# Kernel optimization log

Measured on AMD Instinct MI355X. Metric: run time of the kernel, lower is better.

## Reference

```python
import jax, jax.numpy as jnp
import numpy as np

N, E, B = 4096, 8192, 128


def seg_softmax(logits, seg, n):
    m = jax.ops.segment_max(logits, seg, num_segments=n)
    e = jnp.exp(logits - m[seg])
    s = jax.ops.segment_sum(e, seg, num_segments=n)
    return e / (s[seg] + 1e-16)


def gat(x, src, dst, W, a_src, a_dst, b, H, C, n):
    # PyG GATConv, concat=False (mean over heads), self-loops already appended
    h = (x @ W).reshape(n, H, C)
    al_s = jnp.sum(h * a_src, -1)  # [n,H]
    al_d = jnp.sum(h * a_dst, -1)
    logits = jax.nn.leaky_relu(al_s[src] + al_d[dst], 0.2)  # [E',H]
    alpha = seg_softmax(logits, dst, n)
    out = jax.ops.segment_sum(h[src] * alpha[:, :, None], dst, num_segments=n)
    return out.mean(1) + b


def gcn(x, src, dst, W, b, n):
    deg = jax.ops.segment_sum(jnp.ones_like(dst, jnp.float32), dst, num_segments=n)
    dis = jnp.where(deg > 0, deg ** -0.5, 0.0)
    norm = dis[src] * dis[dst]
    h = x @ W
    return jax.ops.segment_sum(h[src] * norm[:, None], dst, num_segments=n) + b


def transformer_conv(x, src, dst, Wq, bq, Wk, bk, Wv, bv, Ws, bs, H, C, n):
    # PyG TransformerConv, concat=False, root_weight=True, no self-loops
    q = (x @ Wq + bq).reshape(n, H, C)
    k = (x @ Wk + bk).reshape(n, H, C)
    v = (x @ Wv + bv).reshape(n, H, C)
    logits = jnp.sum(q[dst] * k[src], -1) / jnp.sqrt(jnp.float32(C))  # [E,H]
    alpha = seg_softmax(logits, dst, n)
    agg = jax.ops.segment_sum(v[src] * alpha[:, :, None], dst, num_segments=n)
    return agg.mean(1) + (x @ Ws + bs)


def gap(x, batch, nb):
    s = jax.ops.segment_sum(x, batch, num_segments=nb)
    cnt = jax.ops.segment_sum(jnp.ones(x.shape[0], x.dtype), batch, num_segments=nb)
    return s / jnp.maximum(cnt, 1.0)[:, None]


def setup_inputs() -> dict:
    key = jax.random.key(0)
    ks = iter(jax.random.split(key, 64))
    p = {}
    p['x'] = jax.random.normal(next(ks), (N, 78), jnp.float32)
    p['fp'] = (jax.random.uniform(next(ks), (B, 1489)) > 0.5).astype(jnp.float32)
    p['edge_index'] = jax.random.randint(next(ks), (2, E), 0, N, jnp.int32)
    p['batch'] = (jnp.arange(N, dtype=jnp.int32) // (N // B))
    def w(k, shp, fan):
        return jax.random.normal(k, shp, jnp.float32) * (1.0 / np.sqrt(fan))
    # GAT layers (in, out, heads=8)
    for name, ci, co in [('g1', 78, 2048), ('g2', 2048, 1024), ('g3', 1024, 512)]:
        p[name + '_w'] = w(next(ks), (ci, 8 * co), ci)
        p[name + '_as'] = w(next(ks), (8, co), co)
        p[name + '_ad'] = w(next(ks), (8, co), co)
        p[name + '_b'] = jnp.zeros((co,), jnp.float32)
    p['gcn_w'] = w(next(ks), (512, 256), 512)
    p['gcn_b'] = jnp.zeros((256,), jnp.float32)
    # TransformerConv 78->512, heads=4
    for nm in ['t_wq', 't_wk', 't_wv']:
        p[nm] = w(next(ks), (78, 4 * 512), 78)
    for nm in ['t_bq', 't_bk', 't_bv']:
        p[nm] = jnp.zeros((4 * 512,), jnp.float32)
    p['t_ws'] = w(next(ks), (78, 512), 78)
    p['t_bs'] = jnp.zeros((512,), jnp.float32)
    p['fc1_w'] = w(next(ks), (1489, 128), 1489); p['fc1_b'] = jnp.zeros((128,), jnp.float32)
    p['fc2_w'] = w(next(ks), (128, 256), 128); p['fc2_b'] = jnp.zeros((256,), jnp.float32)
    for nm, ci, co in [('b1', 1024, 256), ('b2', 256, 128), ('b3', 128, 64), ('b4', 64, 1)]:
        p[nm + '_w'] = w(next(ks), (ci, co), ci)
        p[nm + '_b'] = jnp.zeros((co,), jnp.float32)
    return p


def reference(x, fp, edge_index, batch,
              g1_w, g1_as, g1_ad, g1_b, g2_w, g2_as, g2_ad, g2_b,
              g3_w, g3_as, g3_ad, g3_b, gcn_w, gcn_b,
              t_wq, t_wk, t_wv, t_bq, t_bk, t_bv, t_ws, t_bs,
              fc1_w, fc1_b, fc2_w, fc2_b,
              b1_w, b1_b, b2_w, b2_b, b3_w, b3_b, b4_w, b4_b):
    n = x.shape[0]
    sl = jnp.arange(n, dtype=edge_index.dtype)
    src_sl = jnp.concatenate([edge_index[0], sl])  # with self loops (GAT/GCN)
    dst_sl = jnp.concatenate([edge_index[1], sl])
    h = jax.nn.relu(gat(x, src_sl, dst_sl, g1_w, g1_as, g1_ad, g1_b, 8, 2048, n))
    h = jax.nn.relu(gat(h, src_sl, dst_sl, g2_w, g2_as, g2_ad, g2_b, 8, 1024, n))
    h = jax.nn.relu(gat(h, src_sl, dst_sl, g3_w, g3_as, g3_ad, g3_b, 8, 512, n))
    h = gcn(h, src_sl, dst_sl, gcn_w, gcn_b, n)
    x_gat = gap(h, batch, B)  # [B,256]
    fpn = jax.nn.relu(fp @ fc1_w + fc1_b)
    fpn = jax.nn.relu(fpn @ fc2_w + fc2_b)  # [B,256]
    xt = jax.nn.relu(transformer_conv(x, edge_index[0], edge_index[1],
                                      t_wq, t_bq, t_wk, t_bk, t_wv, t_bv,
                                      t_ws, t_bs, 4, 512, n))
    x_trans = gap(xt, batch, B)  # [B,512]
    xc = jnp.concatenate([x_gat, x_trans, fpn], axis=1)  # [B,1024]
    h = jax.nn.relu(xc @ b1_w + b1_b)
    h = jax.nn.relu(h @ b2_w + b2_b)
    h = jax.nn.relu(h @ b3_w + b3_b)
    return jax.nn.sigmoid(h @ b4_w + b4_b)
```

## Files before the change

### kernel.cpp

```cpp
#include <hip/hip_runtime.h>

typedef unsigned short u16;
typedef unsigned int   u32;

typedef __bf16 bf16x8 __attribute__((ext_vector_type(8)));
typedef float  f32x4  __attribute__((ext_vector_type(4)));

#define NNODE 4096
#define NEDGE 8192
#define NEG   12288

__device__ __forceinline__ float blo(u32 u){ return __uint_as_float(u<<16); }
__device__ __forceinline__ float bhi(u32 u){ return __uint_as_float(u & 0xffff0000u); }
__device__ __forceinline__ u16 f2b(float f){
  u32 u = __float_as_uint(f);
  u += 0x7fffu + ((u>>16)&1u);
  return (u16)(u>>16);
}
__device__ __forceinline__ void split_bf(float a, u16& hi, u16& lo){
  u32 u = __float_as_uint(a);
  u32 r = u + 0x7fffu + ((u>>16)&1u);
  hi = (u16)(r>>16);
  float h = __uint_as_float(r & 0xffff0000u);
  float l = a - h;
  u32 u2 = __float_as_uint(l);
  lo = (u16)((u2 + 0x7fffu + ((u2>>16)&1u)) >> 16);
}
__device__ __forceinline__ u16 hi_bf(float a){
  u32 u = __float_as_uint(a);
  return (u16)((u + 0x7fffu + ((u>>16)&1u)) >> 16);
}

#define GL2LDS(g,l) __builtin_amdgcn_global_load_lds((const __attribute__((address_space(1))) unsigned int*)(g), (__attribute__((address_space(3))) unsigned int*)(l), 16, 0, 0)

__global__ __launch_bounds__(256) void zero_i(int* p, int n){
  int i = blockIdx.x*256 + threadIdx.x; if (i<n) p[i]=0;
}
__global__ __launch_bounds__(256) void hist_k(const int* __restrict__ ei, int* deg_g, int* deg_t){
  int e = blockIdx.x*256 + threadIdx.x; if (e>=NEG) return;
  int dv = (e<NEDGE) ? ei[NEDGE+e] : e-NEDGE;
  atomicAdd(&deg_g[dv],1);
  if (e<NEDGE) atomicAdd(&deg_t[dv],1);
}
__global__ __launch_bounds__(1024) void scan4096(const int* __restrict__ deg, int* __restrict__ off){
  __shared__ int lds[1024];
  int tid = threadIdx.x;
  int v[4]; int s=0;
  #pragma unroll
  for (int j=0;j<4;j++){ v[j]=deg[tid*4+j]; s+=v[j]; }
  lds[tid]=s; __syncthreads();
  for (int d=1; d<1024; d<<=1){
    int t = (tid>=d) ? lds[tid-d] : 0;
    __syncthreads();
    lds[tid] += t;
    __syncthreads();
  }
  int base = (tid>0) ? lds[tid-1] : 0;
  #pragma unroll
  for (int j=0;j<4;j++){ off[tid*4+j]=base; base+=v[j]; }
  if (tid==1023) off[4096]=base;
}
__global__ __launch_bounds__(256) void scatter_k(const int* __restrict__ ei,
    const int* __restrict__ off_g, int* cur_g, int* csr_g,
    const int* __restrict__ off_t, int* cur_t, int* csr_t){
  int e = blockIdx.x*256 + threadIdx.x; if (e>=NEG) return;
  int s, dv;
  if (e<NEDGE){ s=ei[e]; dv=ei[NEDGE+e]; } else { s=dv=e-NEDGE; }
  int p = atomicAdd(&cur_g[dv],1);
  csr_g[off_g[dv]+p]=s;
  if (e<NEDGE){ int p2 = atomicAdd(&cur_t[dv],1); csr_t[off_t[dv]+p2]=s; }
}
__global__ __launch_bounds__(256) void mkdis(const int* __restrict__ deg, float* dis){
  int i = blockIdx.x*256 + threadIdx.x; if (i>=NNODE) return;
  int d = deg[i]; dis[i] = d>0 ? rsqrtf((float)d) : 0.f;
}
__global__ __launch_bounds__(128) void pad_x(const float* __restrict__ x, float* __restrict__ xp,
                                             u16* __restrict__ xh){
  int n = blockIdx.x, c = threadIdx.x;
  if (c<96){
    float v = (c<78) ? x[(size_t)n*78+c] : 0.f;
    if (c<80) xp[(size_t)n*80+c] = v;
    xh[(size_t)n*96+c] = hi_bf(v);
  }
}
__global__ __launch_bounds__(256) void repack_w1(const float* __restrict__ g1w, float* __restrict__ w1r){
  int i = blockIdx.x*256 + threadIdx.x;
  int kk = i >> 11, c = i & 2047;
  int h = kk/80, k2 = kk - h*80;
  w1r[i] = (k2<78) ? g1w[(size_t)k2*16384 + h*2048 + c] : 0.f;
}

__global__ __launch_bounds__(256) void tpd(const float* __restrict__ in, int Ntot, int n0,
    int K, int Kp, u16* __restrict__ outh){
  __shared__ float t[32][33];
  int bx = blockIdx.x*32;
  int by = blockIdx.y*32;
  int tx = threadIdx.x & 31, ty = threadIdx.x >> 5;
  for (int i=ty;i<32;i+=8){
    int kk=by+i;
    t[i][tx] = (kk<K) ? in[(size_t)kk*Ntot + n0 + bx + tx] : 0.f;
  }
  __syncthreads();
  for (int i=ty;i<32;i+=8){
    int nn=bx+i, kk=by+tx;
    if (kk<Kp) outh[(size_t)nn*Kp+kk] = hi_bf(t[tx][i]);
  }
}

__global__ __launch_bounds__(256) void mk_wsT(const float* __restrict__ wsv, const float* __restrict__ wdv,
    u16* __restrict__ th, u16* __restrict__ tl, int Kp){
  int i = blockIdx.x*256 + threadIdx.x;
  if (i >= 16*Kp) return;
  int r = i / Kp, k = i - r*Kp;
  float v = (r<8) ? wsv[k*8+r] : wdv[k*8+(r-8)];
  u16 h,l; split_bf(v,h,l);
  th[i]=h; tl[i]=l;
}


template<int KS>
__global__ __launch_bounds__(256,4) void alk_mm(
    const u16* __restrict__ Ah, const u16* __restrict__ Al, int lda,
    const u16* __restrict__ Bh, const u16* __restrict__ Bl,
    float* __restrict__ alsd, int K)
{
  __shared__ __align__(16) u16 Ash[128*32], Asl[128*32], Bsh[16*32], Bsl[16*32];
  int tid = threadIdx.x, lane = tid & 63, wave = tid >> 6;
  int bm = blockIdx.y*128;
  int kb = blockIdx.x*(K/KS), ke = kb + K/KS;
  int m16 = lane & 15, quad = lane >> 4;
  int srow = lane >> 2;
  int skk = (((lane & 3) - (srow >> 1)) & 3) * 8;
  int kq  = (((quad + (m16 >> 1)) & 3)) * 8;
  f32x4 acc[2] = {};
  for (int k0=kb; k0<ke; k0+=32){
    __syncthreads();
    #pragma unroll
    for (int t=0;t<2;t++){
      int g = wave + t*4; int row = g*16 + srow;
      GL2LDS(Ah + (size_t)(bm+row)*lda + k0 + skk, &Ash[g*512]);
      GL2LDS(Al + (size_t)(bm+row)*lda + k0 + skk, &Asl[g*512]);
    }
    if (wave==0) GL2LDS(Bh + (size_t)srow*lda + k0 + skk, &Bsh[0]);
    if (wave==1) GL2LDS(Bl + (size_t)srow*lda + k0 + skk, &Bsl[0]);
    __syncthreads();
    bf16x8 bh = *(const bf16x8*)&Bsh[m16*32+kq];
    bf16x8 bl = *(const bf16x8*)&Bsl[m16*32+kq];
    #pragma unroll
    for (int i=0;i<2;i++){
      bf16x8 ah = *(const bf16x8*)&Ash[(wave*32+i*16+m16)*32+kq];
      bf16x8 al = *(const bf16x8*)&Asl[(wave*32+i*16+m16)*32+kq];
      acc[i] = __builtin_amdgcn_mfma_f32_16x16x32_bf16(ah, bh, acc[i],0,0,0);
      acc[i] = __builtin_amdgcn_mfma_f32_16x16x32_bf16(al, bh, acc[i],0,0,0);
      acc[i] = __builtin_amdgcn_mfma_f32_16x16x32_bf16(ah, bl, acc[i],0,0,0);
    }
  }
  #pragma unroll
  for (int i=0;i<2;i++){
    int row0 = bm + wave*32 + i*16 + quad*4;
    #pragma unroll
    for (int r=0;r<4;r++)
      atomicAdd(&alsd[(size_t)(row0+r)*16 + m16], acc[i][r]);
  }
}

#define BM 128
#define BN 128
template<int EPI, int SA, typename CT>
__global__ __launch_bounds__(256,4) void mgemm(
    const u16* __restrict__ Ah, const u16* __restrict__ Al, int lda,
    const u16* __restrict__ Bh, int ldb,
    CT* __restrict__ C, int ldc, int K,
    const float* __restrict__ bias, float scale,
    u16* __restrict__ Chi, u16* __restrict__ Clo)
{
  __shared__ __align__(16) u16 Ash[128*32];
  __shared__ __align__(16) u16 Bsh[128*32];
  __shared__ __align__(16) u16 Asl[SA?128*32:16];
  int tid = threadIdx.x;
  int bm = blockIdx.y*BM, bn = blockIdx.x*BN;
  int lane = tid & 63, wave = tid >> 6;
  int wr = (wave>>1)*64, wc = (wave&1)*64;
  int m16 = lane & 15, quad = lane >> 4;
  int srow = lane >> 2;
  int skk = (((lane & 3) - (srow >> 1)) & 3) * 8;
  int kq  = (((quad + (m16 >> 1)) & 3)) * 8;

  f32x4 acc[4][4] = {};
  for (int k0=0; k0<K; k0+=32){
    __syncthreads();
    #pragma unroll
    for (int t=0;t<2;t++){
      int g = wave + t*4;
      int row = g*16 + srow;
      GL2LDS(Ah + (size_t)(bm+row)*lda + k0 + skk, &Ash[g*512]);
      if (SA) GL2LDS(Al + (size_t)(bm+row)*lda + k0 + skk, &Asl[g*512]);
      GL2LDS(Bh + (size_t)(bn+row)*ldb + k0 + skk, &Bsh[g*512]);
    }
    __syncthreads();
    bf16x8 ah[4], al_[4], bh_[4];
    #pragma unroll
    for (int i=0;i<4;i++){
      ah[i]  = *(const bf16x8*)&Ash[(wr+i*16+m16)*32 + kq];
      if (SA) al_[i] = *(const bf16x8*)&Asl[(wr+i*16+m16)*32 + kq];
    }
    #pragma unroll
    for (int j=0;j<4;j++)
      bh_[j] = *(const bf16x8*)&Bsh[(wc+j*16+m16)*32 + kq];
    #pragma unroll
    for (int i=0;i<4;i++)
      #pragma unroll
      for (int j=0;j<4;j++){
        acc[i][j] = __builtin_amdgcn_mfma_f32_16x16x32_bf16(ah[i], bh_[j], acc[i][j], 0,0,0);
        if (SA) acc[i][j] = __builtin_amdgcn_mfma_f32_16x16x32_bf16(al_[i], bh_[j], acc[i][j], 0,0,0);
      }
  }
  #pragma unroll
  for (int i=0;i<4;i++){
    int row0 = bm + wr + i*16 + quad*4;
    #pragma unroll
    for (int j=0;j<4;j++){
      int col = bn + wc + j*16 + m16;
      float bv = (EPI==1||EPI==5) ? bias[col] : 0.f;
      #pragma unroll
      for (int r=0;r<4;r++){
        float v = acc[i][j][r];
        if constexpr (EPI==5){
          v = fmaxf(v*scale + bv, 0.f);
          size_t idx = (size_t)(row0+r)*ldc + col;
          u16 h_, l_; split_bf(v, h_, l_);
          Chi[idx]=h_; Clo[idx]=l_;
        } else {
          if (EPI==1) v += bv;
          size_t idx = (size_t)(row0+r)*ldc + col;
          if constexpr (sizeof(CT)==2) C[idx] = (CT)f2b(v);
          else C[idx] = (CT)v;
        }
      }
    }
  }
}

__global__ __launch_bounds__(256) void wsvec(const float* __restrict__ W,
    const float* __restrict__ as_, const float* __restrict__ ad_,
    float* __restrict__ ws, float* __restrict__ wd,
    int Kreal, int H, int C)
{
  int wv = blockIdx.x*4 + (threadIdx.x>>6);
  int lane = threadIdx.x & 63;
  int k = wv / H, h = wv - k*H;
  float ps=0.f, pd=0.f;
  if (k < Kreal){
    const float* wr = W + (size_t)k*((size_t)H*C) + (size_t)h*C;
    const float* ar = as_ + (size_t)h*C;
    const float* dr = ad_ + (size_t)h*C;
    for (int c=lane;c<C;c+=64){ float w=wr[c]; ps += w*ar[c]; pd += w*dr[c]; }
  }
  #pragma unroll
  for (int o=32;o;o>>=1){ ps += __shfl_down(ps,o); pd += __shfl_down(pd,o); }
  if (lane==0){ ws[k*H+h]=ps; wd[k*H+h]=pd; }
}
__global__ __launch_bounds__(256) void alk(const float* __restrict__ X,
    const float* __restrict__ ws, const float* __restrict__ wd,
    float* __restrict__ alsd, int Kp)
{
  int n = blockIdx.x, tid = threadIdx.x;
  int hh = tid>>5, l32 = tid&31;
  const float* xr = X + (size_t)n*Kp;
  float ps=0.f, pd=0.f;
  for (int k=l32;k<Kp;k+=32){
    float xv = xr[k];
    ps += xv*ws[k*8+hh];
    pd += xv*wd[k*8+hh];
  }
  #pragma unroll
  for (int o=16;o;o>>=1){ ps += __shfl_down(ps,o,32); pd += __shfl_down(pd,o,32); }
  if (l32==0){ alsd[n*16+hh]=ps; alsd[n*16+8+hh]=pd; }
}

__global__ __launch_bounds__(256) void gat1_gather(
    const float* __restrict__ xpad, const float* __restrict__ alsd,
    const int* __restrict__ off, const int* __restrict__ csr,
    u16* __restrict__ y1h, u16* __restrict__ y1l)
{
  int d = blockIdx.x, tid = threadIdx.x;
  int hh = tid>>5, l32 = tid&31;
  int e0 = off[d], e1 = off[d+1];
  __shared__ float mh[8], lih[8], adh[8];
  __shared__ float wl[32][8];
  __shared__ int sl[32];
  if (tid < 8){
    float ad = alsd[d*16+8+tid]; adh[tid]=ad;
    float m=-1e30f, l=0.f;
    for (int e=e0;e<e1;++e){
      float xv = alsd[csr[e]*16+tid] + ad;
      xv = xv>0.f?xv:0.2f*xv;
      if (xv>m){ l = l*__expf(m-xv)+1.f; m=xv; } else l += __expf(xv-m);
    }
    mh[tid]=m; lih[tid]=1.f/l;
  }
  __syncthreads();
  float acc0=0.f, acc1=0.f, acc2v=0.f;
  for (int cb=e0; cb<e1; cb+=32){
    int ce = min(32, e1-cb);
    if (tid < ce*8){
      int j = tid>>3, h2 = tid&7;
      int s = csr[cb+j];
      if (h2==0) sl[j]=s;
      float xv = alsd[s*16+h2] + adh[h2];
      xv = xv>0.f?xv:0.2f*xv;
      wl[j][h2] = __expf(xv-mh[h2])*lih[h2];
    }
    __syncthreads();
    for (int j=0;j<ce;++j){
      float w = wl[j][hh];
      const float* xr = xpad + (size_t)sl[j]*80;
      acc0 += w*xr[l32];
      acc1 += w*xr[l32+32];
      if (l32 < 16) acc2v += w*xr[l32+64];
    }
    __syncthreads();
  }
  size_t base = (size_t)d*640 + hh*80;
  u16 h_, l_;
  split_bf(acc0, h_, l_); y1h[base+l32]=h_;    y1l[base+l32]=l_;
  split_bf(acc1, h_, l_); y1h[base+l32+32]=h_; y1l[base+l32+32]=l_;
  if (l32<16){ split_bf(acc2v, h_, l_); y1h[base+l32+64]=h_; y1l[base+l32+64]=l_; }
}

template<int HPC, int C>
__global__ __launch_bounds__(256) void gat_aggN(
    const u16* __restrict__ h, const float* __restrict__ alsd,
    const int* __restrict__ off, const int* __restrict__ csr,
    float* __restrict__ accum, int head0)
{
  constexpr int V = C/256;
  int d = blockIdx.x, tid = threadIdx.x;
  int e0=off[d], e1=off[d+1];
  __shared__ float mh[HPC], lih[HPC], adh[HPC];
  __shared__ float wl[32][HPC];
  __shared__ int sl[32];
  if (tid < HPC){
    float ad = alsd[d*16 + 8 + head0 + tid]; adh[tid]=ad;
    float m=-1e30f,l=0.f;
    for (int e=e0;e<e1;++e){
      float xv = alsd[csr[e]*16 + head0 + tid]+ad;
      xv = xv>0.f?xv:0.2f*xv;
      if (xv>m){ l=l*__expf(m-xv)+1.f; m=xv; } else l+=__expf(xv-m);
    }
    mh[tid]=m; lih[tid]=1.f/l;
  }
  __syncthreads();
  float acc[HPC][V];
  #pragma unroll
  for (int a=0;a<HPC;a++)
    #pragma unroll
    for (int v=0;v<V;v++) acc[a][v]=0.f;
  int c0 = tid*V;
  for (int cb=e0;cb<e1;cb+=32){
    int ce = min(32, e1-cb);
    if (tid < ce*HPC){
      int j = tid/HPC, h2 = tid - j*HPC;
      int s = csr[cb+j];
      if (h2==0) sl[j]=s;
      float xv = alsd[s*16 + head0 + h2] + adh[h2];
      xv = xv>0.f?xv:0.2f*xv;
      wl[j][h2] = __expf(xv-mh[h2])*lih[h2];
    }
    __syncthreads();
    for (int j=0;j<ce;++j){
      const u16* hr = h + (size_t)sl[j]*(HPC*C);
      #pragma unroll
      for (int a=0;a<HPC;a++){
        float w = wl[j][a];
        if constexpr (V==4){
          uint2 u = *(const uint2*)(hr + a*C + c0);
          acc[a][0] += w*blo(u.x); acc[a][1] += w*bhi(u.x);
          acc[a][2] += w*blo(u.y); acc[a][3] += w*bhi(u.y);
        } else {
          u32 u = *(const u32*)(hr + a*C + c0);
          acc[a][0] += w*blo(u); acc[a][1] += w*bhi(u);
        }
      }
    }
    __syncthreads();
  }
  float* ar = accum + (size_t)d*C + c0;
  #pragma unroll
  for (int v=0;v<V;v++){
    float s2 = 0.f;
    #pragma unroll
    for (int a=0;a<HPC;a++) s2 += acc[a][v];
    ar[v] += s2;
  }
}
__global__ __launch_bounds__(256) void finishx(const float* __restrict__ accum,
    const float* __restrict__ bias, float* __restrict__ xo, int Cmask){
  int i = blockIdx.x*256 + threadIdx.x;
  int c = i & Cmask;
  xo[i] = fmaxf(accum[i]*0.125f + bias[c], 0.f);
}
__global__ __launch_bounds__(256) void finishx2(const float* __restrict__ accum,
    const float* __restrict__ bias,
    u16* __restrict__ xh, u16* __restrict__ xl, int Cmask){
  int i = blockIdx.x*256 + threadIdx.x;
  int c = i & Cmask;
  float v = fmaxf(accum[i]*0.125f + bias[c], 0.f);
  u16 h_, l_; split_bf(v, h_, l_);
  xh[i]=h_; xl[i]=l_;
}

__global__ __launch_bounds__(256) void pool_gcn(const float* __restrict__ x3,
    const float* __restrict__ dis, const int* __restrict__ off, const int* __restrict__ csr,
    float* __restrict__ z)
{
  int g = blockIdx.x, tid = threadIdx.x;
  int c0 = tid*2;
  float a0=0.f, a1=0.f;
  for (int dd=0; dd<32; ++dd){
    int d = g*32+dd;
    int e0=off[d], e1=off[d+1];
    float b0=0.f, b1=0.f;
    for (int e=e0;e<e1;++e){
      int s = csr[e]; float ds = dis[s];
      const float* xr = x3 + (size_t)s*512 + c0;
      b0 += ds*xr[0]; b1 += ds*xr[1];
    }
    float dw = dis[d];
    a0 += dw*b0; a1 += dw*b1;
  }
  z[(size_t)g*512+c0]   = a0*(1.f/32.f);
  z[(size_t)g*512+c0+1] = a1*(1.f/32.f);
}

__global__ __launch_bounds__(256) void tr_agg(
  const u16* __restrict__ qkvs, const int* __restrict__ off, const int* __restrict__ csr,
  float* __restrict__ xt)
{
  int d = blockIdx.x, tid = threadIdx.x;
  int wv = tid>>6, lane = tid&63;
  int e0=off[d], e1=off[d+1];
  __shared__ float osum[4][512];
  __shared__ float sp[4][64];
  float qf[8];
  { uint4 u = *(const uint4*)(qkvs + (size_t)d*6656 + wv*512 + lane*8);
    qf[0]=blo(u.x); qf[1]=bhi(u.x); qf[2]=blo(u.y); qf[3]=bhi(u.y);
    qf[4]=blo(u.z); qf[5]=bhi(u.z); qf[6]=blo(u.w); qf[7]=bhi(u.w); }
  const float scale = 0.04419417382415922f;
  float m=-1e30f,l=0.f;
  for (int e=e0;e<e1;++e){
    int s = csr[e];
    uint4 u = *(const uint4*)(qkvs + (size_t)s*6656 + 2048 + wv*512 + lane*8);
    float p = qf[0]*blo(u.x)+qf[1]*bhi(u.x)+qf[2]*blo(u.y)+qf[3]*bhi(u.y)
            + qf[4]*blo(u.z)+qf[5]*bhi(u.z)+qf[6]*blo(u.w)+qf[7]*bhi(u.w);
    #pragma unroll
    for (int o=32;o;o>>=1) p += __shfl_xor(p,o);
    p *= scale;
    int idx = e-e0;
    if (lane==0 && idx<64) sp[wv][idx]=p;
    if (p>m){ l=l*__expf(m-p)+1.f; m=p; } else l+=__expf(p-m);
  }
  float li = (e1>e0)?1.f/l:0.f;
  float acc[8]={0.f,0.f,0.f,0.f,0.f,0.f,0.f,0.f};
  for (int e=e0;e<e1;++e){
    int s = csr[e];
    int idx = e-e0;
    float p;
    if (idx<64) p = sp[wv][idx];
    else {
      uint4 u = *(const uint4*)(qkvs + (size_t)s*6656 + 2048 + wv*512 + lane*8);
      p = qf[0]*blo(u.x)+qf[1]*bhi(u.x)+qf[2]*blo(u.y)+qf[3]*bhi(u.y)
        + qf[4]*blo(u.z)+qf[5]*bhi(u.z)+qf[6]*blo(u.w)+qf[7]*bhi(u.w);
      #pragma unroll
      for (int o=32;o;o>>=1) p += __shfl_xor(p,o);
      p *= scale;
    }
    float w = __expf(p - m)*li;
    uint4 u = *(const uint4*)(qkvs + (size_t)s*6656 + 4096 + wv*512 + lane*8);
    acc[0]+=w*blo(u.x); acc[1]+=w*bhi(u.x); acc[2]+=w*blo(u.y); acc[3]+=w*bhi(u.y);
    acc[4]+=w*blo(u.z); acc[5]+=w*bhi(u.z); acc[6]+=w*blo(u.w); acc[7]+=w*bhi(u.w);
  }
  #pragma unroll
  for (int j=0;j<8;j++) osum[wv][lane*8+j]=acc[j];
  __syncthreads();
  for (int c=tid;c<512;c+=256){
    u16 sk = qkvs[(size_t)d*6656 + 6144 + c];
    float o = (osum[0][c]+osum[1][c]+osum[2][c]+osum[3][c])*0.25f + blo((u32)sk);
    xt[(size_t)d*512+c] = fmaxf(o,0.f);
  }
}

__global__ __launch_bounds__(256) void catb(const float* __restrict__ bq, const float* __restrict__ bk,
    const float* __restrict__ bv, const float* __restrict__ bs, float* __restrict__ o){
  int i = blockIdx.x*256 + threadIdx.x; if (i>=6656) return;
  float v;
  if (i<2048) v=bq[i]; else if (i<4096) v=bk[i-2048];
  else if (i<6144) v=bv[i-4096]; else v=bs[i-6144];
  o[i]=v;
}

__device__ __forceinline__ float dotb(const u16* __restrict__ w, const float* __restrict__ s,
                                      int k0, int k1){
  float acc=0.f;
  #pragma unroll 4
  for (int k=k0;k<k1;k+=8){
    uint4 u = *(const uint4*)(w+k);
    float4 s0 = *(const float4*)(s+k);
    float4 s1 = *(const float4*)(s+k+4);
    acc += blo(u.x)*s0.x + bhi(u.x)*s0.y + blo(u.y)*s0.z + bhi(u.y)*s0.w
         + blo(u.z)*s1.x + bhi(u.z)*s1.y + blo(u.w)*s1.z + bhi(u.w)*s1.w;
  }
  return acc;
}
__global__ __launch_bounds__(256) void head_k(
  const float* __restrict__ z, const float* __restrict__ xt, const float* __restrict__ fp,
  const u16* __restrict__ gcnT, const float* __restrict__ gcn_b,
  const u16* __restrict__ fc1T, const float* __restrict__ fc1_b,
  const u16* __restrict__ fc2T, const float* __restrict__ fc2_b,
  const u16* __restrict__ b1T, const float* __restrict__ b1_b,
  const u16* __restrict__ b2T, const float* __restrict__ b2_b,
  const u16* __restrict__ b3T, const float* __restrict__ b3_b,
  const float* __restrict__ b4_w, const float* __restrict__ b4_b,
  float* __restrict__ out)
{
  int g = blockIdx.x, tid = threadIdx.x;
  __shared__ __align__(16) float xc[1024];
  __shared__ __align__(16) float sa[1504];
  __shared__ __align__(16) float sb[256];
  __shared__ __align__(16) float scm[256];
  for (int c=tid;c<512;c+=256) sa[c] = z[(size_t)g*512+c];
  __syncthreads();
  float vgcn = gcn_b[tid] + dotb(gcnT + (size_t)tid*512, sa, 0, 512);
  for (int c=tid;c<512;c+=256){
    float s=0.f;
    for (int i=0;i<32;i++) s += xt[(size_t)(g*32+i)*512 + c];
    xc[256+c] = s*(1.f/32.f);
  }
  xc[tid] = vgcn;
  __syncthreads();
  for (int c=tid;c<1496;c+=256) sa[c] = (c<1489) ? fp[(size_t)g*1489+c] : 0.f;
  __syncthreads();
  { int n = tid & 127, half = tid >> 7;
    sb[tid] = dotb(fc1T + (size_t)n*1496, sa, half?752:0, half?1496:752); }
  __syncthreads();
  if (tid<128) scm[tid] = fmaxf(sb[tid]+sb[tid+128]+fc1_b[tid], 0.f);
  __syncthreads();
  xc[768+tid] = fmaxf(fc2_b[tid] + dotb(fc2T + (size_t)tid*128, scm, 0, 128), 0.f);
  __syncthreads();
  sa[tid] = fmaxf(b1_b[tid] + dotb(b1T + (size_t)tid*1024, xc, 0, 1024), 0.f);
  __syncthreads();
  { int n = tid & 127, half = tid >> 7;
    sb[tid] = dotb(b2T + (size_t)n*256, sa, half*128, half*128+128); }
  __syncthreads();
  if (tid<128) scm[tid] = fmaxf(sb[tid]+sb[tid+128]+b2_b[tid], 0.f);
  __syncthreads();
  { int n = tid & 63, part = tid >> 6;
    sb[tid] = dotb(b3T + (size_t)n*128, scm, part*32, part*32+32); }
  __syncthreads();
  if (tid<64) sa[tid] = fmaxf(sb[tid]+sb[tid+64]+sb[tid+128]+sb[tid+192]+b3_b[tid], 0.f);
  __syncthreads();
  if (tid<64){
    float p = sa[tid]*b4_w[tid];
    #pragma unroll
    for (int o=32;o;o>>=1) p += __shfl_down(p,o);
    if (tid==0) out[g] = 1.f/(1.f+__expf(-(p + b4_b[0])));
  }
}

extern "C" void kernel_launch(void* const* d_in, const int* in_sizes, int n_in,
                              void* d_out, int out_size, void* d_ws, size_t ws_size,
                              hipStream_t stream)
{
  (void)in_sizes; (void)n_in; (void)out_size; (void)ws_size;
  const float* x     = (const float*)d_in[0];
  const float* fp    = (const float*)d_in[1];
  const int*   ei    = (const int*)d_in[2];
  const float* g1_w  = (const float*)d_in[4];
  const float* g1_as = (const float*)d_in[5];
  const float* g1_ad = (const float*)d_in[6];
  const float* g1_b  = (const float*)d_in[7];
  const float* g2_w  = (const float*)d_in[8];
  const float* g2_as = (const float*)d_in[9];
  const float* g2_ad = (const float*)d_in[10];
  const float* g2_b  = (const float*)d_in[11];
  const float* g3_w  = (const float*)d_in[12];
  const float* g3_as = (const float*)d_in[13];
  const float* g3_ad = (const float*)d_in[14];
  const float* g3_b  = (const float*)d_in[15];
  const float* gcn_w = (const float*)d_in[16];
  const float* gcn_b = (const float*)d_in[17];
  const float* t_wq  = (const float*)d_in[18];
  const float* t_wk  = (const float*)d_in[19];
  const float* t_wv  = (const float*)d_in[20];
  const float* t_bq  = (const float*)d_in[21];
  const float* t_bk  = (const float*)d_in[22];
  const float* t_bv  = (const float*)d_in[23];
  const float* t_ws  = (const float*)d_in[24];
  const float* t_bs  = (const float*)d_in[25];
  const float* fc1_w = (const float*)d_in[26];
  const float* fc1_b = (const float*)d_in[27];
  const float* fc2_w = (const float*)d_in[28];
  const float* fc2_b = (const float*)d_in[29];
  const float* b1_w  = (const float*)d_in[30];
  const float* b1_b  = (const float*)d_in[31];
  const float* b2_w  = (const float*)d_in[32];
  const float* b2_b  = (const float*)d_in[33];
  const float* b3_w  = (const float*)d_in[34];
  const float* b3_b  = (const float*)d_in[35];
  const float* b4_w  = (const float*)d_in[36];
  const float* b4_b  = (const float*)d_in[37];

  char* base = (char*)d_ws;
  size_t offb = 0;
  auto alloc = [&](size_t bytes)->void*{
    void* p = base + offb; offb = (offb + bytes + 255) & ~(size_t)255; return p;
  };
  int*   cnt   = (int*)alloc(16384*4);
  int*   off_g = (int*)alloc(4097*4);
  int*   off_t = (int*)alloc(4097*4);
  int*   csr_g = (int*)alloc(12288*4);
  int*   csr_t = (int*)alloc(8192*4);
  float* dis   = (float*)alloc(4096*4);
  float* xpad  = (float*)alloc((size_t)4096*80*4);
  u16*   xph   = (u16*)alloc((size_t)4096*96*2);
  float* alsd  = (float*)alloc((size_t)4096*16*4);
  float* wsv   = (float*)alloc((size_t)2048*8*4);
  float* wdv   = (float*)alloc((size_t)2048*8*4);
  u16*   wsTh  = (u16*)alloc((size_t)16*2048*2);
  u16*   wsTl  = (u16*)alloc((size_t)16*2048*2);
  float* zbuf  = (float*)alloc((size_t)128*512*4);
  float* cbias = (float*)alloc((size_t)6656*4);
  float* w1r   = (float*)alloc((size_t)640*2048*4);
  u16*   gcnT  = (u16*)alloc((size_t)256*512*2);
  u16*   fc1T  = (u16*)alloc((size_t)128*1496*2);
  u16*   fc2T  = (u16*)alloc((size_t)256*128*2);
  u16*   b1T   = (u16*)alloc((size_t)256*1024*2);
  u16*   b2T   = (u16*)alloc((size_t)128*256*2);
  u16*   b3T   = (u16*)alloc((size_t)64*128*2);
  char*  big   = (char*)alloc((size_t)140<<20);

  u16*   y1h   = (u16*)  (big);
  u16*   y1l   = (u16*)  (big + ((size_t)5<<20));
  u16*   w1rth = (u16*)  (big + ((size_t)10<<20));
  u16*   x1h   = (u16*)  (big + ((size_t)16<<20));
  u16*   x1l   = (u16*)  (big + ((size_t)32<<20));
  u16*   w2th  = (u16*)  (big + ((size_t)48<<20));
  u16*   h2    = (u16*)  (big + ((size_t)64<<20));
  float* acc2  = (float*)(big + ((size_t)96<<20));
  u16*   x2h   = (u16*)  (big + ((size_t)112<<20));
  u16*   x2l   = (u16*)  (big + ((size_t)120<<20));
  u16*   w3th  = (u16*)  (big);
  u16*   h3    = (u16*)  (big + ((size_t)8<<20));
  float* acc3  = (float*)(big + ((size_t)40<<20));
  float* x3    = (float*)(big + ((size_t)48<<20));
  u16*   qkvTh = (u16*)  (big);
  u16*   qkvs  = (u16*)  (big + ((size_t)8<<20));
  float* xt    = (float*)(big + ((size_t)64<<20));

  int* deg_g = cnt;       int* cur_g = cnt+4096;
  int* deg_t = cnt+8192;  int* cur_t = cnt+12288;

  zero_i<<<64,256,0,stream>>>(cnt, 16384);
  hist_k<<<48,256,0,stream>>>(ei, deg_g, deg_t);
  scan4096<<<1,1024,0,stream>>>(deg_g, off_g);
  scan4096<<<1,1024,0,stream>>>(deg_t, off_t);
  scatter_k<<<48,256,0,stream>>>(ei, off_g, cur_g, csr_g, off_t, cur_t, csr_t);
  mkdis<<<16,256,0,stream>>>(deg_g, dis);
  pad_x<<<4096,128,0,stream>>>(x, xpad, xph);
  repack_w1<<<5120,256,0,stream>>>(g1_w, w1r);
  tpd<<<dim3(8,16),256,0,stream>>>(gcn_w, 256, 0, 512, 512, gcnT);
  tpd<<<dim3(4,47),256,0,stream>>>(fc1_w, 128, 0, 1489, 1496, fc1T);
  tpd<<<dim3(8,4), 256,0,stream>>>(fc2_w, 256, 0, 128, 128, fc2T);
  tpd<<<dim3(8,32),256,0,stream>>>(b1_w,  256, 0, 1024, 1024, b1T);
  tpd<<<dim3(4,8), 256,0,stream>>>(b2_w,  128, 0, 256, 256, b2T);
  tpd<<<dim3(2,4), 256,0,stream>>>(b3_w,  64,  0, 128, 128, b3T);

  wsvec<<<160,256,0,stream>>>(g1_w, g1_as, g1_ad, wsv, wdv, 78, 8, 2048);
  alk<<<4096,256,0,stream>>>(xpad, wsv, wdv, alsd, 80);
  gat1_gather<<<4096,256,0,stream>>>(xpad, alsd, off_g, csr_g, y1h, y1l);
  tpd<<<dim3(64,20),256,0,stream>>>(w1r, 2048, 0, 640, 640, w1rth);
  mgemm<5,1,float><<<dim3(16,32),256,0,stream>>>(y1h, y1l, 640, w1rth, 640,
                                         nullptr, 2048, 640, g1_b, 0.125f, x1h, x1l);

  wsvec<<<4096,256,0,stream>>>(g2_w, g2_as, g2_ad, wsv, wdv, 2048, 8, 1024);
  mk_wsT<<<128,256,0,stream>>>(wsv, wdv, wsTh, wsTl, 2048);
  hipMemsetAsync(alsd, 0, (size_t)4096*16*4, stream);
  alk_mm<8><<<dim3(8,32),256,0,stream>>>(x1h, x1l, 2048, wsTh, wsTl, alsd, 2048);
  hipMemsetAsync(acc2, 0, (size_t)4096*1024*4, stream);
  for (int c=0;c<2;c++){
    tpd<<<dim3(128,64),256,0,stream>>>(g2_w, 8192, c*4096, 2048, 2048, w2th);
    mgemm<0,0,u16><<<dim3(32,32),256,0,stream>>>(x1h, nullptr, 2048, w2th, 2048,
                                           h2, 4096, 2048, nullptr, 0.f, nullptr, nullptr);
    gat_aggN<4,1024><<<4096,256,0,stream>>>(h2, alsd, off_g, csr_g, acc2, c*4);
  }
  finishx2<<<16384,256,0,stream>>>(acc2, g2_b, x2h, x2l, 1023);

  wsvec<<<2048,256,0,stream>>>(g3_w, g3_as, g3_ad, wsv, wdv, 1024, 8, 512);
  mk_wsT<<<64,256,0,stream>>>(wsv, wdv, wsTh, wsTl, 1024);
  hipMemsetAsync(alsd, 0, (size_t)4096*16*4, stream);
  alk_mm<8><<<dim3(8,32),256,0,stream>>>(x2h, x2l, 1024, wsTh, wsTl, alsd, 1024);
  hipMemsetAsync(acc3, 0, (size_t)4096*512*4, stream);
  tpd<<<dim3(128,32),256,0,stream>>>(g3_w, 4096, 0, 1024, 1024, w3th);
  mgemm<0,0,u16><<<dim3(32,32),256,0,stream>>>(x2h, nullptr, 1024, w3th, 1024,
                                         h3, 4096, 1024, nullptr, 0.f, nullptr, nullptr);
  gat_aggN<8,512><<<4096,256,0,stream>>>(h3, alsd, off_g, csr_g, acc3, 0);
  finishx<<<8192,256,0,stream>>>(acc3, g3_b, x3, 511);
  pool_gcn<<<128,256,0,stream>>>(x3, dis, off_g, csr_g, zbuf);

  tpd<<<dim3(64,3),256,0,stream>>>(t_wq, 2048, 0, 78, 96, qkvTh);
  tpd<<<dim3(64,3),256,0,stream>>>(t_wk, 2048, 0, 78, 96, qkvTh + (size_t)2048*96);
  tpd<<<dim3(64,3),256,0,stream>>>(t_wv, 2048, 0, 78, 96, qkvTh + (size_t)4096*96);
  tpd<<<dim3(16,3),256,0,stream>>>(t_ws, 512,  0, 78, 96, qkvTh + (size_t)6144*96);
  catb<<<26,256,0,stream>>>(t_bq, t_bk, t_bv, t_bs, cbias);
  mgemm<1,0,u16><<<dim3(52,32),256,0,stream>>>(xph, nullptr, 96, qkvTh, 96,
                                         qkvs, 6656, 96, cbias, 0.f, nullptr, nullptr);
  tr_agg<<<4096,256,0,stream>>>(qkvs, off_t, csr_t, xt);

  head_k<<<128,256,0,stream>>>(zbuf, xt, fp, gcnT, gcn_b,
                               fc1T, fc1_b, fc2T, fc2_b,
                               b1T, b1_b, b2T, b2_b, b3T, b3_b, b4_w, b4_b,
                               (float*)d_out);
}
```

Before: 781.8 us.

## Add 256x256-tile 8-wave pipelined bf16 GEMM for GAT layer 2/3 projections

Introduces mgemm8, a 512-thread kernel computing 256x256 output tiles with double-buffered LDS loaded by direct global-to-LDS copies, swizzled LDS addressing, interleaved MFMA/load phases with s_setprio, and an XCD-aware block remap. It replaces the previous 128-class mgemm for the large GAT layer 2 and 3 feature GEMMs. The aim is higher MFMA utilisation and more operand reuse per tile. In exchange it uses 128KB of LDS per block and relies on hand-placed waitcnt values, and it assumes dimensions divisible by 256 and an even number of K tiles.

Result: slower. 828.7 us (+6.0%).

```diff
diff --git a/kernel.cpp b/kernel.cpp
--- a/kernel.cpp
+++ b/kernel.cpp
@@ -237,6 +237,130 @@
           else C[idx] = (CT)v;
         }
       }
+    }
+  }
+}
+
+__device__ __forceinline__ void stA8(const u16* __restrict__ A, int lda, u16* dst,
+                                     int bm, int kt, int h, int w, int lane){
+  #pragma unroll
+  for (int t=0;t<2;t++){
+    int rbase = t*128 + h*64 + w*8;
+    int rl = rbase + (lane>>3);
+    int q = ((lane&7) - ((rl&15)>>1)) & 7;
+    GL2LDS(A + (size_t)(bm+rl)*lda + kt*64 + q*8, dst + rbase*64);
+  }
+}
+__device__ __forceinline__ void stB8(const u16* __restrict__ B, int ldb, u16* dst,
+                                     int bn, int kt, int nh, int w, int lane){
+  #pragma unroll
+  for (int t=0;t<2;t++){
+    int rbase = (w>>1)*64 + nh*32 + (w&1)*16 + t*8;
+    int rl = rbase + (lane>>3);
+    int q = ((lane&7) - ((rl&15)>>1)) & 7;
+    GL2LDS(B + (size_t)(bn+rl)*ldb + kt*64 + q*8, dst + rbase*64);
+  }
+}
+#define LDX8(BUF, ROW, KS) \
+  (*(const bf16x8*)&(BUF)[(ROW)*64 + ((((KS)*4 + quad + (m16>>1)) & 7))*8])
+#define RDA8(BUF, MH) \
+  _Pragma("unroll") for (int mi=0;mi<4;mi++){ \
+    a_[mi][0] = LDX8(BUF, wr*128 + ((MH)*4+mi)*16 + m16, 0); \
+    a_[mi][1] = LDX8(BUF, wr*128 + ((MH)*4+mi)*16 + m16, 1); }
+#define RDB8(BUF, NH, BB) \
+  _Pragma("unroll") for (int nj=0;nj<2;nj++){ \
+    BB[nj][0] = LDX8(BUF, wc*64 + ((NH)*2+nj)*16 + m16, 0); \
+    BB[nj][1] = LDX8(BUF, wc*64 + ((NH)*2+nj)*16 + m16, 1); }
+#define MMQ8(MH, NH, BB) \
+  _Pragma("unroll") for (int mi=0;mi<4;mi++) \
+    _Pragma("unroll") for (int nj=0;nj<2;nj++){ \
+      acc[(MH)*4+mi][(NH)*2+nj] = __builtin_amdgcn_mfma_f32_16x16x32_bf16(a_[mi][0], BB[nj][0], acc[(MH)*4+mi][(NH)*2+nj],0,0,0); \
+      acc[(MH)*4+mi][(NH)*2+nj] = __builtin_amdgcn_mfma_f32_16x16x32_bf16(a_[mi][1], BB[nj][1], acc[(MH)*4+mi][(NH)*2+nj],0,0,0); }
+#define LGKM0 asm volatile("s_waitcnt lgkmcnt(0)" ::: "memory")
+#define BAR   __builtin_amdgcn_s_barrier()
+
+__global__ __launch_bounds__(512,2) void mgemm8(
+    const u16* __restrict__ A, int lda,
+    const u16* __restrict__ B, int ldb,
+    u16* __restrict__ C, int ldc, int K, int nbx)
+{
+  __shared__ __align__(16) u16 As0[16384], As1[16384], Bs0[16384], Bs1[16384];
+  int tid = threadIdx.x, lane = tid & 63, w = tid >> 6;
+  int m16 = lane & 15, quad = lane >> 4;
+  int wr = w >> 2, wc = w & 3;
+  int nwg = (int)gridDim.x, bid = (int)blockIdx.x;
+  int wg = (bid & 7)*(nwg>>3) + (bid>>3);
+  int by = wg / nbx, bx = wg - by*nbx;
+  int bm = by*256, bn = bx*256;
+  int NT = K >> 6, NP = NT >> 1;
+  f32x4 acc[8][4] = {};
+  bf16x8 a_[4][2], b0_[2][2], b1_[2][2];
+  stA8(A,lda,As0,bm,0,0,w,lane);
+  stB8(B,ldb,Bs0,bn,0,0,w,lane);
+  stB8(B,ldb,Bs0,bn,0,1,w,lane);
+  stA8(A,lda,As0,bm,0,1,w,lane);
+  stA8(A,lda,As1,bm,1,0,w,lane);
+  stB8(B,ldb,Bs1,bn,1,0,w,lane);
+  stB8(B,ldb,Bs1,bn,1,1,w,lane);
+  stA8(A,lda,As1,bm,1,1,w,lane);
+  asm volatile("s_waitcnt vmcnt(8)" ::: "memory");
+  BAR;
+  for (int i=0;i<NP;i++){
+    int t2 = 2*i+2; if (t2>=NT) t2=NT-1;
+    int t3 = 2*i+3; if (t3>=NT) t3=NT-1;
+    RDA8(As0,0); RDB8(Bs0,0,b0_);
+    asm volatile("s_waitcnt lgkmcnt(8)" ::: "memory");
+    BAR; LGKM0;
+    __builtin_amdgcn_s_setprio(1); MMQ8(0,0,b0_); __builtin_amdgcn_s_setprio(0);
+    BAR;
+    RDB8(Bs0,1,b1_);
+    stA8(A,lda,As0,bm,t2,0,w,lane);
+    stB8(B,ldb,Bs0,bn,t2,0,w,lane);
+    BAR; LGKM0;
+    __builtin_amdgcn_s_setprio(1); MMQ8(0,1,b1_); __builtin_amdgcn_s_setprio(0);
+    BAR;
+    RDA8(As0,1);
+    stB8(B,ldb,Bs0,bn,t2,1,w,lane);
+    BAR; LGKM0;
+    __builtin_amdgcn_s_setprio(1); MMQ8(1,1,b1_); __builtin_amdgcn_s_setprio(0);
+    BAR;
+    stA8(A,lda,As0,bm,t2,1,w,lane);
+    BAR;
+    __builtin_amdgcn_s_setprio(1); MMQ8(1,0,b0_); __builtin_amdgcn_s_setprio(0);
+    asm volatile("s_waitcnt vmcnt(8)" ::: "memory");
+    BAR;
+    RDA8(As1,0); RDB8(Bs1,0,b0_);
+    asm volatile("s_waitcnt lgkmcnt(8)" ::: "memory");
+    BAR; LGKM0;
+    __builtin_amdgcn_s_setprio(1); MMQ8(0,0,b0_); __builtin_amdgcn_s_setprio(0);
+    BAR;
+    RDB8(Bs1,1,b1_);
+    stA8(A,lda,As1,bm,t3,0,w,lane);
+    stB8(B,ldb,Bs1,bn,t3,0,w,lane);
+    BAR; LGKM0;
+    __builtin_amdgcn_s_setprio(1); MMQ8(0,1,b1_); __builtin_amdgcn_s_setprio(0);
+    BAR;
+    RDA8(As1,1);
+    stB8(B,ldb,Bs1,bn,t3,1,w,lane);
+    BAR; LGKM0;
+    __builtin_amdgcn_s_setprio(1); MMQ8(1,1,b1_); __builtin_amdgcn_s_setprio(0);
+    BAR;
+    stA8(A,lda,As1,bm,t3,1,w,lane);
+    BAR;
+    __builtin_amdgcn_s_setprio(1); MMQ8(1,0,b0_); __builtin_amdgcn_s_setprio(0);
+    asm volatile("s_waitcnt vmcnt(8)" ::: "memory");
+    BAR;
+  }
+  asm volatile("s_waitcnt vmcnt(0)" ::: "memory");
+  #pragma unroll
+  for (int mi=0;mi<8;mi++){
+    int row0 = bm + wr*128 + mi*16 + quad*4;
+    #pragma unroll
+    for (int nj=0;nj<4;nj++){
+      int col = bn + wc*64 + nj*16 + m16;
+      #pragma unroll
+      for (int r=0;r<4;r++)
+        C[(size_t)(row0+r)*ldc + col] = f2b(acc[mi][nj][r]);
     }
   }
 }
@@ -689,8 +813,7 @@
   hipMemsetAsync(acc2, 0, (size_t)4096*1024*4, stream);
   for (int c=0;c<2;c++){
     tpd<<<dim3(128,64),256,0,stream>>>(g2_w, 8192, c*4096, 2048, 2048, w2th);
-    mgemm<0,0,u16><<<dim3(32,32),256,0,stream>>>(x1h, nullptr, 2048, w2th, 2048,
-                                           h2, 4096, 2048, nullptr, 0.f, nullptr, nullptr);
+    mgemm8<<<256,512,0,stream>>>(x1h, 2048, w2th, 2048, h2, 4096, 2048, 16);
     gat_aggN<4,1024><<<4096,256,0,stream>>>(h2, alsd, off_g, csr_g, acc2, c*4);
   }
   finishx2<<<16384,256,0,stream>>>(acc2, g2_b, x2h, x2l, 1023);
@@ -701,8 +824,7 @@
   alk_mm<8><<<dim3(8,32),256,0,stream>>>(x2h, x2l, 1024, wsTh, wsTl, alsd, 1024);
   hipMemsetAsync(acc3, 0, (size_t)4096*512*4, stream);
   tpd<<<dim3(128,32),256,0,stream>>>(g3_w, 4096, 0, 1024, 1024, w3th);
-  mgemm<0,0,u16><<<dim3(32,32),256,0,stream>>>(x2h, nullptr, 1024, w3th, 1024,
-                                         h3, 4096, 1024, nullptr, 0.f, nullptr, nullptr);
+  mgemm8<<<256,512,0,stream>>>(x2h, 1024, w3th, 1024, h3, 4096, 1024, 16);
   gat_aggN<8,512><<<4096,256,0,stream>>>(h3, alsd, off_g, csr_g, acc3, 0);
   finishx<<<8192,256,0,stream>>>(acc3, g3_b, x3, 511);
   pool_gcn<<<128,256,0,stream>>>(x3, dis, off_g, csr_g, zbuf);
```
